# Optimization experiments

Hardware: AMD Instinct MI355X
Metric: run time of the kernel (lower is better)

Reference implementation:

```python
import jax, jax.numpy as jnp
import numpy as np

DIM = 256
HEADS = 4
DEPTH = DIM // HEADS
EXPAND = 4
EPS = 1e-3  # keras BatchNormalization default epsilon


def _bn(x, gamma, beta, mean, var):
    # inference-mode batch norm over last axis
    return gamma * (x - mean) * jax.lax.rsqrt(var + EPS) + beta


def setup_inputs() -> dict:
    key = jax.random.key(0)
    ks = jax.random.split(key, 12)
    B, S, D = 4, 2048, DIM
    H = D * EXPAND
    s = 1.0 / np.sqrt(D)
    inp = {
        "x": jax.random.normal(ks[0], (B, S, D), jnp.float32),
        "bn1_gamma": jnp.ones((D,), jnp.float32),
        "bn1_beta": jnp.zeros((D,), jnp.float32),
        "bn1_mean": jax.random.normal(ks[1], (D,), jnp.float32) * 0.1,
        "bn1_var": jnp.abs(jax.random.normal(ks[2], (D,), jnp.float32)) + 0.5,
        "wq": jax.random.normal(ks[3], (D, D), jnp.float32) * s,
        "bq": jnp.zeros((D,), jnp.float32),
        "wk": jax.random.normal(ks[4], (D, D), jnp.float32) * s,
        "bk": jnp.zeros((D,), jnp.float32),
        "wv": jax.random.normal(ks[5], (D, D), jnp.float32) * s,
        "bv": jnp.zeros((D,), jnp.float32),
        "wo": jax.random.normal(ks[6], (D, D), jnp.float32) * s,
        "bo": jnp.zeros((D,), jnp.float32),
        "bn2_gamma": jnp.ones((D,), jnp.float32),
        "bn2_beta": jnp.zeros((D,), jnp.float32),
        "bn2_mean": jax.random.normal(ks[7], (D,), jnp.float32) * 0.1,
        "bn2_var": jnp.abs(jax.random.normal(ks[8], (D,), jnp.float32)) + 0.5,
        "w1": jax.random.normal(ks[9], (D, H), jnp.float32) * s,
        "w2": jax.random.normal(ks[10], (H, D), jnp.float32) * (1.0 / np.sqrt(H)),
    }
    return inp


def reference(x, bn1_gamma, bn1_beta, bn1_mean, bn1_var,
              wq, bq, wk, bk, wv, bv, wo, bo,
              bn2_gamma, bn2_beta, bn2_mean, bn2_var, w1, w2):
    B, S, D = x.shape
    h = _bn(x, bn1_gamma, bn1_beta, bn1_mean, bn1_var)
    # project and split heads -> [B, H, S, depth]
    def heads(t):
        return t.reshape(B, S, HEADS, DEPTH).transpose(0, 2, 1, 3)
    q = heads(h @ wq + bq)
    k = heads(h @ wk + bk)
    v = heads(h @ wv + bv)
    scores = jnp.einsum("bhqd,bhkd->bhqk", q, k) / jnp.sqrt(jnp.float32(DEPTH))
    attn = jax.nn.softmax(scores, axis=-1)
    ctx = jnp.einsum("bhqk,bhkd->bhqd", attn, v)
    ctx = ctx.transpose(0, 2, 1, 3).reshape(B, S, D)
    attn_out = ctx @ wo + bo
    x1 = attn_out + x  # residual (dropout = identity at inference)
    h2 = _bn(x1, bn2_gamma, bn2_beta, bn2_mean, bn2_var)
    m = jax.nn.gelu(h2 @ w1, approximate=False) @ w2
    return m + x1
```

## Files before the change

### kernel.cpp

```cpp
#include <hip/hip_runtime.h>

typedef unsigned short u16;
typedef unsigned int u32;
typedef short short8 __attribute__((ext_vector_type(8)));
typedef short short4v __attribute__((ext_vector_type(4)));
typedef float f32x4 __attribute__((ext_vector_type(4)));

#define EPS 1e-3f
#define C1F 0.18033688011112042f

#if defined(__HIP_DEVICE_COMPILE__)
#define MFMA16(a, b, c) __builtin_amdgcn_mfma_f32_16x16x16bf16_1k(a, b, c, 0, 0, 0)
#define EXP2F(x) __builtin_amdgcn_exp2f(x)
#else
#define MFMA16(a, b, c) (c)
#define EXP2F(x) exp2f(x)
#endif

static __device__ __forceinline__ u16 f2bf(float f) {
    u32 u = __float_as_uint(f);
    u += 0x7fffu + ((u >> 16) & 1u);
    return (u16)(u >> 16);
}
static __device__ __forceinline__ float bf2f(u16 v) {
    u32 u = (u32)v << 16;
    return __uint_as_float(u);
}
static __device__ __forceinline__ u32 pack_bf2_trunc(float a, float b) {
    return __builtin_amdgcn_perm(__float_as_uint(b), __float_as_uint(a), 0x07060302u);
}
static __device__ __forceinline__ void async_cp16(const void* g, void* l) {
    __builtin_amdgcn_global_load_lds(
        (const __attribute__((address_space(1))) unsigned int*)g,
        (__attribute__((address_space(3))) unsigned int*)l, 16, 0, 0);
}

__global__ void prep_bn1_kernel(const float* __restrict__ x,
                            const float* __restrict__ wq, const float* __restrict__ wk,
                            const float* __restrict__ wv, const float* __restrict__ wo,
                            const float* __restrict__ w1, const float* __restrict__ w2,
                            const float* __restrict__ bq, const float* __restrict__ bk,
                            const float* __restrict__ bv,
                            const float* __restrict__ g1, const float* __restrict__ b1,
                            const float* __restrict__ m1, const float* __restrict__ v1,
                            const float* __restrict__ g2, const float* __restrict__ b2,
                            const float* __restrict__ m2, const float* __restrict__ v2,
                            u16* __restrict__ h,
                            u16* __restrict__ wqkvT, u16* __restrict__ woT,
                            u16* __restrict__ w1T, u16* __restrict__ w2T,
                            float* __restrict__ bqkv,
                            float* __restrict__ bn2sc, float* __restrict__ bn2sh) {
    int bid = blockIdx.x;
    if (bid < 2048) {
        int idx = bid * 256 + threadIdx.x;
        int base = idx * 4;
        int c = base & 255;
        float4 xv = *(const float4*)(x + base);
        ushort4 pk;
        {
            float sc0 = g1[c] * rsqrtf(v1[c] + EPS);
            pk.x = f2bf(fmaf(xv.x, sc0, b1[c] - m1[c] * sc0));
            float sc1 = g1[c+1] * rsqrtf(v1[c+1] + EPS);
            pk.y = f2bf(fmaf(xv.y, sc1, b1[c+1] - m1[c+1] * sc1));
            float sc2 = g1[c+2] * rsqrtf(v1[c+2] + EPS);
            pk.z = f2bf(fmaf(xv.z, sc2, b1[c+2] - m1[c+2] * sc2));
            float sc3 = g1[c+3] * rsqrtf(v1[c+3] + EPS);
            pk.w = f2bf(fmaf(xv.w, sc3, b1[c+3] - m1[c+3] * sc3));
        }
        *(ushort4*)(h + base) = pk;
        return;
    }
    int idx = (bid - 2048) * 256 + threadIdx.x;
    if (idx < 196608) {
        int sec = idx >> 16;
        int i = idx & 65535;
        int k = i >> 8, n = i & 255;
        const float* w = sec == 0 ? wq : (sec == 1 ? wk : wv);
        float v = w[i];
        if (sec == 1) v *= C1F;
        wqkvT[(sec * 256 + n) * 256 + k] = f2bf(v);
    } else if (idx < 262144) {
        int i = idx - 196608; int k = i >> 8, n = i & 255;
        woT[n * 256 + k] = f2bf(wo[i]);
    } else if (idx < 524288) {
        int i = idx - 262144; int k = i >> 10, n = i & 1023;
        w1T[n * 256 + k] = f2bf(w1[i]);
    } else if (idx < 786432) {
        int i = idx - 524288; int k = i >> 8, n = i & 255;
        w2T[n * 1024 + k] = f2bf(w2[i]);
    } else if (idx < 787200) {
        int i = idx - 786432;
        bqkv[i] = (i < 256) ? bq[i] : (i < 512 ? bk[i - 256] * C1F : bv[i - 512]);
    } else if (idx < 787456) {
        int i = idx - 787200;
        float sc = g2[i] * rsqrtf(v2[i] + EPS);
        bn2sc[i] = sc; bn2sh[i] = b2[i] - m2[i] * sc;
    }
}

template <int EPI>
__global__ __launch_bounds__(256) void gemm128(
        const u16* __restrict__ A, const u16* __restrict__ Bt,
        int M, int N, int K,
        const float* __restrict__ bias, u16* __restrict__ out_bf,
        u16* __restrict__ out_vt) {
    __shared__ u16 abuf[2][4096];
    __shared__ u16 bbuf[2][8192];
    const int t = threadIdx.x;
    const int w = t >> 6, lane = t & 63;
    const int l = lane & 15, Q = lane >> 4;
    const int m0 = blockIdx.x * 64;
    const int n0 = blockIdx.y * 128;
    const int rh = (w & 1) * 32;
    const int ch = (w >> 1) * 64;

    f32x4 acc[2][4];
#pragma unroll
    for (int mt = 0; mt < 2; ++mt)
#pragma unroll
        for (int nt = 0; nt < 4; ++nt) acc[mt][nt] = (f32x4){0.f, 0.f, 0.f, 0.f};

    auto stage = [&](int k0, int b) {
#pragma unroll
        for (int j = 0; j < 2; ++j) {
            int idx = j * 256 + t;
            int r = idx >> 3, c8 = idx & 7;
            int sc = c8 ^ (r & 7);
            async_cp16(A + (size_t)(m0 + r) * K + k0 + sc * 8, abuf[b] + idx * 8);
        }
#pragma unroll
        for (int j = 0; j < 4; ++j) {
            int idx = j * 256 + t;
            int r = idx >> 3, c8 = idx & 7;
            int sc = c8 ^ (r & 7);
            async_cp16(Bt + (size_t)(n0 + r) * K + k0 + sc * 8, bbuf[b] + idx * 8);
        }
    };

    const int nit = K >> 6;
    stage(0, 0);
    for (int i = 0; i < nit; ++i) {
        __syncthreads();
        if (i + 1 < nit) stage((i + 1) << 6, (i + 1) & 1);
        const u16* ab = abuf[i & 1];
        const u16* bb = bbuf[i & 1];
#pragma unroll
        for (int kd = 0; kd < 2; ++kd) {
            short8 afr[2], bfr[4];
#pragma unroll
            for (int mt = 0; mt < 2; ++mt) {
                int ar = rh + mt * 16 + l;
                afr[mt] = *(const short8*)(ab + ar * 64 + (((kd * 4 + Q) ^ (ar & 7))) * 8);
            }
#pragma unroll
            for (int nt = 0; nt < 4; ++nt) {
                int br = ch + nt * 16 + l;
                bfr[nt] = *(const short8*)(bb + br * 64 + (((kd * 4 + Q) ^ (br & 7))) * 8);
            }
#pragma unroll
            for (int mt = 0; mt < 2; ++mt)
#pragma unroll
                for (int nt = 0; nt < 4; ++nt)
                    acc[mt][nt] = __builtin_amdgcn_mfma_f32_16x16x32_bf16(afr[mt], bfr[nt], acc[mt][nt], 0, 0, 0);
        }
    }

#pragma unroll
    for (int mt = 0; mt < 2; ++mt)
#pragma unroll
        for (int nt = 0; nt < 4; ++nt) {
            int col = n0 + ch + nt * 16 + l;
            int row0 = m0 + rh + mt * 16 + Q * 4;
            if (EPI == 0) {
                float b = bias[col];
                if (col < 512) {
#pragma unroll
                    for (int r = 0; r < 4; ++r)
                        out_bf[(size_t)(row0 + r) * 512 + col] = f2bf(acc[mt][nt][r] + b);
                } else {
                    ushort4 pk;
                    pk.x = f2bf(acc[mt][nt][0] + b);
                    pk.y = f2bf(acc[mt][nt][1] + b);
                    pk.z = f2bf(acc[mt][nt][2] + b);
                    pk.w = f2bf(acc[mt][nt][3] + b);
                    *(ushort4*)(out_vt + (size_t)(col - 512) * 8192 + row0) = pk;
                }
            } else {
#pragma unroll
                for (int r = 0; r < 4; ++r) {
                    float val = acc[mt][nt][r];
                    float gl = 0.5f * val * (1.f + erff(val * 0.70710678118654752f));
                    out_bf[(size_t)(row0 + r) * N + col] = f2bf(gl);
                }
            }
        }
}

__global__ __launch_bounds__(256) void gemm64_res(
        const u16* __restrict__ A, const u16* __restrict__ Bt,
        int M, int N, int K,
        const float* __restrict__ resid, float* __restrict__ out_f32) {
    __shared__ u16 abuf[2][4096];
    __shared__ u16 bbuf[2][4096];
    const int t = threadIdx.x;
    const int w = t >> 6, lane = t & 63;
    const int l = lane & 15, Q = lane >> 4;
    const int m0 = blockIdx.x * 64;
    const int n0 = blockIdx.y * 64;

    f32x4 acc[4];
#pragma unroll
    for (int nt = 0; nt < 4; ++nt) acc[nt] = (f32x4){0.f, 0.f, 0.f, 0.f};

    auto stage = [&](int k0, int b) {
#pragma unroll
        for (int j = 0; j < 2; ++j) {
            int idx = j * 256 + t;
            int r = idx >> 3, c8 = idx & 7;
            int sc = c8 ^ (r & 7);
            async_cp16(A + (size_t)(m0 + r) * K + k0 + sc * 8, abuf[b] + idx * 8);
        }
#pragma unroll
        for (int j = 0; j < 2; ++j) {
            int idx = j * 256 + t;
            int r = idx >> 3, c8 = idx & 7;
            int sc = c8 ^ (r & 7);
            async_cp16(Bt + (size_t)(n0 + r) * K + k0 + sc * 8, bbuf[b] + idx * 8);
        }
    };

    const int nit = K >> 6;
    stage(0, 0);
    for (int i = 0; i < nit; ++i) {
        __syncthreads();
        if (i + 1 < nit) stage((i + 1) << 6, (i + 1) & 1);
        const u16* ab = abuf[i & 1];
        const u16* bb = bbuf[i & 1];
#pragma unroll
        for (int kd = 0; kd < 2; ++kd) {
            int ar = w * 16 + l;
            short8 afr = *(const short8*)(ab + ar * 64 + (((kd * 4 + Q) ^ (ar & 7))) * 8);
#pragma unroll
            for (int nt = 0; nt < 4; ++nt) {
                int r = nt * 16 + l;
                short8 bfr = *(const short8*)(bb + r * 64 + (((kd * 4 + Q) ^ (r & 7))) * 8);
                acc[nt] = __builtin_amdgcn_mfma_f32_16x16x32_bf16(afr, bfr, acc[nt], 0, 0, 0);
            }
        }
    }

#pragma unroll
    for (int nt = 0; nt < 4; ++nt) {
        int col = n0 + nt * 16 + l;
        int row0 = m0 + w * 16 + Q * 4;
#pragma unroll
        for (int r = 0; r < 4; ++r) {
            size_t oidx = (size_t)(row0 + r) * N + col;
            out_f32[oidx] = acc[nt][r] + resid[oidx];
        }
    }
}

__global__ __launch_bounds__(256) void gemm_oproj(
        const u16* __restrict__ opart, const float* __restrict__ lpart,
        const u16* __restrict__ Bt,
        const float* __restrict__ bias, const float* __restrict__ resid,
        float* __restrict__ out_f32, u16* __restrict__ out_bf,
        const float* __restrict__ b2sc, const float* __restrict__ b2sh) {
    __shared__ u16 abuf[4096];
    __shared__ u16 bbuf[2][4096];
    const int t = threadIdx.x;
    const int w = t >> 6, lane = t & 63;
    const int l = lane & 15, Q = lane >> 4;
    const int m0 = blockIdx.x * 64;
    const int n0 = blockIdx.y * 64;
    const size_t SPSTR = (size_t)16 * 2048 * 64;

    f32x4 acc[4];
#pragma unroll
    for (int nt = 0; nt < 4; ++nt) acc[nt] = (f32x4){0.f, 0.f, 0.f, 0.f};

    auto stageB = [&](int k0, int b) {
#pragma unroll
        for (int j = 0; j < 2; ++j) {
            int idx = j * 256 + t;
            int r = idx >> 3, c8 = idx & 7;
            int sc = c8 ^ (r & 7);
            async_cp16(Bt + (size_t)(n0 + r) * 256 + k0 + sc * 8, bbuf[b] + idx * 8);
        }
    };

    stageB(0, 0);
    for (int i = 0; i < 4; ++i) {
        uint4 aw[2];
#pragma unroll
        for (int j = 0; j < 2; ++j) {
            int idx = j * 256 + t;
            int r = idx >> 3, c8 = idx & 7;
            int dc = c8 ^ (r & 7);
            int row = m0 + r;
            int bh = (row >> 11) * 4 + i;
            int q = row & 2047;
            size_t lb = (size_t)bh * 2048 + q;
            float ls = lpart[lb] + lpart[lb + 32768] + lpart[lb + 65536] + lpart[lb + 98304];
            float inv = 1.0f / ls;
            size_t base = ((size_t)bh * 2048 + q) * 64 + dc * 8;
            uint4 v0 = *(const uint4*)(opart + base);
            uint4 v1 = *(const uint4*)(opart + SPSTR + base);
            uint4 v2 = *(const uint4*)(opart + 2 * SPSTR + base);
            uint4 v3 = *(const uint4*)(opart + 3 * SPSTR + base);
            u32 o[4];
            const u32* p0 = &v0.x; const u32* p1 = &v1.x;
            const u32* p2 = &v2.x; const u32* p3 = &v3.x;
#pragma unroll
            for (int e = 0; e < 4; ++e) {
                float lo = __uint_as_float(p0[e] << 16) + __uint_as_float(p1[e] << 16)
                         + __uint_as_float(p2[e] << 16) + __uint_as_float(p3[e] << 16);
                float hi = __uint_as_float(p0[e] & 0xffff0000u) + __uint_as_float(p1[e] & 0xffff0000u)
                         + __uint_as_float(p2[e] & 0xffff0000u) + __uint_as_float(p3[e] & 0xffff0000u);
                o[e] = (u32)f2bf(lo * inv) | ((u32)f2bf(hi * inv) << 16);
            }
            aw[j] = make_uint4(o[0], o[1], o[2], o[3]);
        }
        __syncthreads();
#pragma unroll
        for (int j = 0; j < 2; ++j)
            *(uint4*)(abuf + ((size_t)(j * 256 + t)) * 8) = aw[j];
        if (i < 3) stageB((i + 1) * 64, (i + 1) & 1);
        __syncthreads();
        const u16* bb = bbuf[i & 1];
#pragma unroll
        for (int kd = 0; kd < 2; ++kd) {
            int ar = w * 16 + l;
            short8 afr = *(const short8*)(abuf + ar * 64 + (((kd * 4 + Q) ^ (ar & 7))) * 8);
#pragma unroll
            for (int nt = 0; nt < 4; ++nt) {
                int r = nt * 16 + l;
                short8 bfr = *(const short8*)(bb + r * 64 + (((kd * 4 + Q) ^ (r & 7))) * 8);
                acc[nt] = __builtin_amdgcn_mfma_f32_16x16x32_bf16(afr, bfr, acc[nt], 0, 0, 0);
            }
        }
    }

#pragma unroll
    for (int nt = 0; nt < 4; ++nt) {
        int col = n0 + nt * 16 + l;
        int row0 = m0 + w * 16 + Q * 4;
#pragma unroll
        for (int r = 0; r < 4; ++r) {
            size_t oidx = (size_t)(row0 + r) * 256 + col;
            float val = acc[nt][r] + bias[col] + resid[oidx];
            out_f32[oidx] = val;
            out_bf[oidx] = f2bf(fmaf(val, b2sc[col], b2sh[col]));
        }
    }
}

static __device__ __forceinline__ void stage_tiles(const u16* kglob, const u16* vglob,
                                                   u16* kdst, u16* vdst,
                                                   int w, int lane, int kt) {
#pragma unroll
    for (int j = 0; j < 2; ++j) {
        int cw = (w * 2 + j) * 64 + lane;
        int r = cw >> 3;
        int c = (cw & 7) ^ (r & 7);
        async_cp16(kglob + ((size_t)(kt * 64 + r)) * 512 + c * 8, kdst + (w * 2 + j) * 512);
        async_cp16(vglob + ((size_t)r) * 8192 + kt * 64 + c * 8, vdst + (w * 2 + j) * 512);
    }
}

__global__ __launch_bounds__(256) void attn_kernel(const u16* __restrict__ qk,
                                                   const u16* __restrict__ vT,
                                                   u16* __restrict__ opart,
                                                   float* __restrict__ lpart) {
    __shared__ u16 kbuf[2][4096];
    __shared__ u16 vbuf[2][4096];
    const int t = threadIdx.x;
    const int w = t >> 6, lane = t & 63;
    const int l = lane & 15, Q = lane >> 4;
    const int blk = blockIdx.x;
    const int qt = blk >> 6;
    const int sp = (blk >> 4) & 3;
    const int bh = blk & 15;
    const int bb = bh >> 2, hd = bh & 3;
    const size_t rowbase = (size_t)bb * 2048;
    const int q0 = qt * 128 + w * 32;

    short8 qf[2][2];
#pragma unroll
    for (int g = 0; g < 2; ++g)
#pragma unroll
        for (int kd = 0; kd < 2; ++kd)
            qf[g][kd] = *(const short8*)(qk + (rowbase + q0 + g * 16 + l) * 512
                                         + hd * 64 + kd * 32 + Q * 8);

    f32x4 o[2][4];
#pragma unroll
    for (int g = 0; g < 2; ++g)
#pragma unroll
        for (int dt = 0; dt < 4; ++dt) o[g][dt] = (f32x4){0.f, 0.f, 0.f, 0.f};
    f32x4 oL[2];
    oL[0] = (f32x4){0.f, 0.f, 0.f, 0.f};
    oL[1] = (f32x4){0.f, 0.f, 0.f, 0.f};
    union { u32 u[2]; short4v s4; } ones;
    ones.u[0] = 0x3F803F80u; ones.u[1] = 0x3F803F80u;

    const u16* kglob = qk + (rowbase + sp * 512) * 512 + 256 + hd * 64;
    const u16* vglob = vT + ((size_t)(hd * 64)) * 8192 + rowbase + sp * 512;

    stage_tiles(kglob, vglob, kbuf[0], vbuf[0], w, lane, 0);
    for (int kt = 0; kt < 8; ++kt) {
        __syncthreads();
        if (kt + 1 < 8)
            stage_tiles(kglob, vglob, kbuf[(kt + 1) & 1], vbuf[(kt + 1) & 1],
                        w, lane, kt + 1);
        const u16* kb = kbuf[kt & 1];
        const u16* vb = vbuf[kt & 1];

        union { u32 u[2]; short4v s4; } pf[2][4];
#pragma unroll
        for (int st = 0; st < 4; ++st) {
            int r = st * 16 + l;
            short8 kf0 = *(const short8*)(kb + r * 64 + ((Q) ^ (r & 7)) * 8);
            short8 kf1 = *(const short8*)(kb + r * 64 + ((4 + Q) ^ (r & 7)) * 8);
#pragma unroll
            for (int g = 0; g < 2; ++g) {
                f32x4 s = (f32x4){0.f, 0.f, 0.f, 0.f};
                s = __builtin_amdgcn_mfma_f32_16x16x32_bf16(kf0, qf[g][0], s, 0, 0, 0);
                s = __builtin_amdgcn_mfma_f32_16x16x32_bf16(kf1, qf[g][1], s, 0, 0, 0);
                float p0 = EXP2F(s[0]);
                float p1 = EXP2F(s[1]);
                float p2 = EXP2F(s[2]);
                float p3 = EXP2F(s[3]);
                pf[g][st].u[0] = pack_bf2_trunc(p0, p1);
                pf[g][st].u[1] = pack_bf2_trunc(p2, p3);
            }
        }

#pragma unroll
        for (int c = 0; c < 4; ++c) {
#pragma unroll
            for (int dt = 0; dt < 4; ++dt) {
                int r = dt * 16 + l;
                int slot = (2 * c + (Q >> 1)) ^ (r & 7);
                short4v vf = *(const short4v*)(vb + r * 64 + slot * 8 + (Q & 1) * 4);
                o[0][dt] = MFMA16(vf, pf[0][c].s4, o[0][dt]);
                o[1][dt] = MFMA16(vf, pf[1][c].s4, o[1][dt]);
            }
            oL[0] = MFMA16(ones.s4, pf[0][c].s4, oL[0]);
            oL[1] = MFMA16(ones.s4, pf[1][c].s4, oL[1]);
        }
    }

#pragma unroll
    for (int g = 0; g < 2; ++g) {
        u16* ob = opart + (((size_t)sp * 16 + bh) * 2048 + q0 + g * 16) * 64;
#pragma unroll
        for (int dt = 0; dt < 4; ++dt) {
            ushort4 pk;
            pk.x = f2bf(o[g][dt][0]);
            pk.y = f2bf(o[g][dt][1]);
            pk.z = f2bf(o[g][dt][2]);
            pk.w = f2bf(o[g][dt][3]);
            *(ushort4*)(ob + (size_t)l * 64 + dt * 16 + Q * 4) = pk;
        }
        if (Q == 0) {
            size_t lb = ((size_t)sp * 16 + bh) * 2048 + q0 + g * 16;
            lpart[lb + l] = oL[g][0];
        }
    }
}

extern "C" void kernel_launch(void* const* d_in, const int* in_sizes, int n_in,
                              void* d_out, int out_size, void* d_ws, size_t ws_size,
                              hipStream_t stream) {
    (void)in_sizes; (void)n_in; (void)out_size; (void)ws_size;
    const float* x  = (const float*)d_in[0];
    const float* g1 = (const float*)d_in[1];
    const float* b1 = (const float*)d_in[2];
    const float* m1 = (const float*)d_in[3];
    const float* v1 = (const float*)d_in[4];
    const float* wq = (const float*)d_in[5];
    const float* bq = (const float*)d_in[6];
    const float* wk = (const float*)d_in[7];
    const float* bk = (const float*)d_in[8];
    const float* wv = (const float*)d_in[9];
    const float* bv = (const float*)d_in[10];
    const float* wo = (const float*)d_in[11];
    const float* bo = (const float*)d_in[12];
    const float* g2 = (const float*)d_in[13];
    const float* b2 = (const float*)d_in[14];
    const float* m2 = (const float*)d_in[15];
    const float* v2 = (const float*)d_in[16];
    const float* w1 = (const float*)d_in[17];
    const float* w2 = (const float*)d_in[18];

    char* ws = (char*)d_ws;
    u16*   qkb    = (u16*)(ws + (0ull << 20));
    u16*   vTb    = (u16*)(ws + (8ull << 20));
    u16*   h_buf  = (u16*)(ws + (12ull << 20));
    float* x1     = (float*)(ws + (20ull << 20));
    u16*   h2     = (u16*)(ws + (28ull << 20));
    u16*   gbuf   = (u16*)(ws + (32ull << 20));
    u16*   opart  = (u16*)(ws + (48ull << 20));
    float* lpart  = (float*)(ws + (80ull << 20));
    u16*   wqkvT  = (u16*)(ws + (81ull << 20));
    u16*   woT    = (u16*)(ws + (82ull << 20));
    u16*   w1T    = (u16*)(ws + (83ull << 20));
    u16*   w2T    = (u16*)(ws + (84ull << 20));
    float* bqkv   = (float*)(ws + (85ull << 20));
    float* bn2sc  = (float*)(ws + (85ull << 20) + 4096);
    float* bn2sh  = (float*)(ws + (85ull << 20) + 8192);
    float* out    = (float*)d_out;

    prep_bn1_kernel<<<5125, 256, 0, stream>>>(x, wq, wk, wv, wo, w1, w2, bq, bk, bv,
                                              g1, b1, m1, v1, g2, b2, m2, v2,
                                              h_buf, wqkvT, woT, w1T, w2T, bqkv,
                                              bn2sc, bn2sh);
    gemm128<0><<<dim3(128, 6), 256, 0, stream>>>(
        h_buf, wqkvT, 8192, 768, 256, bqkv, qkb, vTb);
    attn_kernel<<<1024, 256, 0, stream>>>(qkb, vTb, opart, lpart);
    gemm_oproj<<<dim3(128, 4), 256, 0, stream>>>(
        opart, lpart, woT, bo, x, x1, h2, bn2sc, bn2sh);
    gemm128<2><<<dim3(128, 8), 256, 0, stream>>>(
        h2, w1T, 8192, 1024, 256, bqkv, gbuf, nullptr);
    gemm64_res<<<dim3(128, 4), 256, 0, stream>>>(
        gbuf, w2T, 8192, 256, 1024, x1, out);
}
```

Measured before the change: 178.3 us.

## Retile N=256 GEMMs to 16-row blocks covering full output width

The output projection and second FFN GEMM now give each block 16 rows and all 256 output columns, with each warp owning 64 columns, in place of 64x64 tiles. Each A row (including the costly split-attention reduction in the o-proj) is therefore loaded and reduced once rather than four times across column blocks. The cost is that every block stages the full 256x64 weight slice per k-step (32 KB per buffer), which raises shared-memory use and weight traffic from L2. The attention kernel's V-fragment read also now indexes the double buffer directly by kt.

```diff
diff --git a/kernel.cpp b/kernel.cpp
--- a/kernel.cpp
+++ b/kernel.cpp
@@ -196,53 +196,47 @@
         }
 }
 
-__global__ __launch_bounds__(256) void gemm64_res(
+__global__ __launch_bounds__(256) void gemm_ffn2(
         const u16* __restrict__ A, const u16* __restrict__ Bt,
-        int M, int N, int K,
         const float* __restrict__ resid, float* __restrict__ out_f32) {
-    __shared__ u16 abuf[2][4096];
-    __shared__ u16 bbuf[2][4096];
+    __shared__ u16 abuf[2][1024];
+    __shared__ u16 bbuf[2][16384];
     const int t = threadIdx.x;
     const int w = t >> 6, lane = t & 63;
     const int l = lane & 15, Q = lane >> 4;
-    const int m0 = blockIdx.x * 64;
-    const int n0 = blockIdx.y * 64;
+    const int m0 = blockIdx.x * 16;
 
     f32x4 acc[4];
 #pragma unroll
     for (int nt = 0; nt < 4; ++nt) acc[nt] = (f32x4){0.f, 0.f, 0.f, 0.f};
 
     auto stage = [&](int k0, int b) {
-#pragma unroll
-        for (int j = 0; j < 2; ++j) {
+        if (t < 128) {
+            int r = t >> 3, c8 = t & 7;
+            int sc = c8 ^ (r & 7);
+            async_cp16(A + (size_t)(m0 + r) * 1024 + k0 + sc * 8, abuf[b] + t * 8);
+        }
+#pragma unroll
+        for (int j = 0; j < 8; ++j) {
             int idx = j * 256 + t;
             int r = idx >> 3, c8 = idx & 7;
             int sc = c8 ^ (r & 7);
-            async_cp16(A + (size_t)(m0 + r) * K + k0 + sc * 8, abuf[b] + idx * 8);
-        }
-#pragma unroll
-        for (int j = 0; j < 2; ++j) {
-            int idx = j * 256 + t;
-            int r = idx >> 3, c8 = idx & 7;
-            int sc = c8 ^ (r & 7);
-            async_cp16(Bt + (size_t)(n0 + r) * K + k0 + sc * 8, bbuf[b] + idx * 8);
+            async_cp16(Bt + (size_t)r * 1024 + k0 + sc * 8, bbuf[b] + idx * 8);
         }
     };
 
-    const int nit = K >> 6;
     stage(0, 0);
-    for (int i = 0; i < nit; ++i) {
+    for (int i = 0; i < 16; ++i) {
         __syncthreads();
-        if (i + 1 < nit) stage((i + 1) << 6, (i + 1) & 1);
+        if (i + 1 < 16) stage((i + 1) << 6, (i + 1) & 1);
         const u16* ab = abuf[i & 1];
         const u16* bb = bbuf[i & 1];
 #pragma unroll
         for (int kd = 0; kd < 2; ++kd) {
-            int ar = w * 16 + l;
-            short8 afr = *(const short8*)(ab + ar * 64 + (((kd * 4 + Q) ^ (ar & 7))) * 8);
+            short8 afr = *(const short8*)(ab + l * 64 + (((kd * 4 + Q) ^ (l & 7))) * 8);
 #pragma unroll
             for (int nt = 0; nt < 4; ++nt) {
-                int r = nt * 16 + l;
+                int r = w * 64 + nt * 16 + l;
                 short8 bfr = *(const short8*)(bb + r * 64 + (((kd * 4 + Q) ^ (r & 7))) * 8);
                 acc[nt] = __builtin_amdgcn_mfma_f32_16x16x32_bf16(afr, bfr, acc[nt], 0, 0, 0);
             }
@@ -251,11 +245,11 @@
 
 #pragma unroll
     for (int nt = 0; nt < 4; ++nt) {
-        int col = n0 + nt * 16 + l;
-        int row0 = m0 + w * 16 + Q * 4;
+        int col = w * 64 + nt * 16 + l;
+        int row0 = m0 + Q * 4;
 #pragma unroll
         for (int r = 0; r < 4; ++r) {
-            size_t oidx = (size_t)(row0 + r) * N + col;
+            size_t oidx = (size_t)(row0 + r) * 256 + col;
             out_f32[oidx] = acc[nt][r] + resid[oidx];
         }
     }
@@ -267,13 +261,12 @@
         const float* __restrict__ bias, const float* __restrict__ resid,
         float* __restrict__ out_f32, u16* __restrict__ out_bf,
         const float* __restrict__ b2sc, const float* __restrict__ b2sh) {
-    __shared__ u16 abuf[4096];
-    __shared__ u16 bbuf[2][4096];
+    __shared__ u16 abuf[1024];
+    __shared__ u16 bbuf[2][16384];
     const int t = threadIdx.x;
     const int w = t >> 6, lane = t & 63;
     const int l = lane & 15, Q = lane >> 4;
-    const int m0 = blockIdx.x * 64;
-    const int n0 = blockIdx.y * 64;
+    const int m0 = blockIdx.x * 16;
     const size_t SPSTR = (size_t)16 * 2048 * 64;
 
     f32x4 acc[4];
@@ -282,21 +275,19 @@
 
     auto stageB = [&](int k0, int b) {
 #pragma unroll
-        for (int j = 0; j < 2; ++j) {
+        for (int j = 0; j < 8; ++j) {
             int idx = j * 256 + t;
             int r = idx >> 3, c8 = idx & 7;
             int sc = c8 ^ (r & 7);
-            async_cp16(Bt + (size_t)(n0 + r) * 256 + k0 + sc * 8, bbuf[b] + idx * 8);
+            async_cp16(Bt + (size_t)r * 256 + k0 + sc * 8, bbuf[b] + idx * 8);
         }
     };
 
     stageB(0, 0);
     for (int i = 0; i < 4; ++i) {
-        uint4 aw[2];
-#pragma unroll
-        for (int j = 0; j < 2; ++j) {
-            int idx = j * 256 + t;
-            int r = idx >> 3, c8 = idx & 7;
+        uint4 aw;
+        if (t < 128) {
+            int r = t >> 3, c8 = t & 7;
             int dc = c8 ^ (r & 7);
             int row = m0 + r;
             int bh = (row >> 11) * 4 + i;
@@ -320,22 +311,20 @@
                          + __uint_as_float(p2[e] & 0xffff0000u) + __uint_as_float(p3[e] & 0xffff0000u);
                 o[e] = (u32)f2bf(lo * inv) | ((u32)f2bf(hi * inv) << 16);
             }
-            aw[j] = make_uint4(o[0], o[1], o[2], o[3]);
+            aw = make_uint4(o[0], o[1], o[2], o[3]);
         }
         __syncthreads();
-#pragma unroll
-        for (int j = 0; j < 2; ++j)
-            *(uint4*)(abuf + ((size_t)(j * 256 + t)) * 8) = aw[j];
+        if (t < 128)
+            *(uint4*)(abuf + (size_t)t * 8) = aw;
         if (i < 3) stageB((i + 1) * 64, (i + 1) & 1);
         __syncthreads();
         const u16* bb = bbuf[i & 1];
 #pragma unroll
         for (int kd = 0; kd < 2; ++kd) {
-            int ar = w * 16 + l;
-            short8 afr = *(const short8*)(abuf + ar * 64 + (((kd * 4 + Q) ^ (ar & 7))) * 8);
+            short8 afr = *(const short8*)(abuf + l * 64 + (((kd * 4 + Q) ^ (l & 7))) * 8);
 #pragma unroll
             for (int nt = 0; nt < 4; ++nt) {
-                int r = nt * 16 + l;
+                int r = w * 64 + nt * 16 + l;
                 short8 bfr = *(const short8*)(bb + r * 64 + (((kd * 4 + Q) ^ (r & 7))) * 8);
                 acc[nt] = __builtin_amdgcn_mfma_f32_16x16x32_bf16(afr, bfr, acc[nt], 0, 0, 0);
             }
@@ -344,8 +333,8 @@
 
 #pragma unroll
     for (int nt = 0; nt < 4; ++nt) {
-        int col = n0 + nt * 16 + l;
-        int row0 = m0 + w * 16 + Q * 4;
+        int col = w * 64 + nt * 16 + l;
+        int row0 = m0 + Q * 4;
 #pragma unroll
         for (int r = 0; r < 4; ++r) {
             size_t oidx = (size_t)(row0 + r) * 256 + col;
@@ -443,7 +432,7 @@
             for (int dt = 0; dt < 4; ++dt) {
                 int r = dt * 16 + l;
                 int slot = (2 * c + (Q >> 1)) ^ (r & 7);
-                short4v vf = *(const short4v*)(vb + r * 64 + slot * 8 + (Q & 1) * 4);
+                short4v vf = *(const short4v*)(vbuf[kt & 1] + r * 64 + slot * 8 + (Q & 1) * 4);
                 o[0][dt] = MFMA16(vf, pf[0][c].s4, o[0][dt]);
                 o[1][dt] = MFMA16(vf, pf[1][c].s4, o[1][dt]);
             }
@@ -520,10 +509,10 @@
     gemm128<0><<<dim3(128, 6), 256, 0, stream>>>(
         h_buf, wqkvT, 8192, 768, 256, bqkv, qkb, vTb);
     attn_kernel<<<1024, 256, 0, stream>>>(qkb, vTb, opart, lpart);
-    gemm_oproj<<<dim3(128, 4), 256, 0, stream>>>(
+    gemm_oproj<<<512, 256, 0, stream>>>(
         opart, lpart, woT, bo, x, x1, h2, bn2sc, bn2sh);
     gemm128<2><<<dim3(128, 8), 256, 0, stream>>>(
         h2, w1T, 8192, 1024, 256, bqkv, gbuf, nullptr);
-    gemm64_res<<<dim3(128, 4), 256, 0, stream>>>(
-        gbuf, w2T, 8192, 256, 1024, x1, out);
-}
+    gemm_ffn2<<<512, 256, 0, stream>>>(
+        gbuf, w2T, x1, out);
+}
```

New measurement: 185.5 us. 1.04x slower.
